# Kernel tuning notes

Hardware: AMD Instinct MI355X
Metric: run time of the kernel (lower is better)

## Reference

```python
import jax, jax.numpy as jnp
import numpy as np


def _softsign(x):
    return x / (1.0 + jnp.abs(x))


def _pad_conv3d(x, w, b):
    # replicate-pad by 1 on each spatial side, then VALID 3x3x3 conv (NCDHW)
    x = jnp.pad(x, ((0, 0), (0, 0), (1, 1), (1, 1), (1, 1)), mode='edge')
    y = jax.lax.conv_general_dilated(
        x, w, window_strides=(1, 1, 1), padding='VALID',
        dimension_numbers=('NCDHW', 'OIDHW', 'NCDHW'))
    return y + b[None, :, None, None, None]


N_MID = 100  # number of 1->1 conv blocks


def setup_inputs() -> dict:
    key = jax.random.key(0)
    ks = jax.random.split(key, 8)
    B, S = 16, 64
    preop = jax.random.normal(ks[0], (B, 1, S, S, S), dtype=jnp.float32)
    intraop = jax.random.normal(ks[1], (B, 1, S, S, S), dtype=jnp.float32)
    # conv weights: PyTorch-style kaiming-ish scale for 3x3x3 kernels
    w0 = jax.random.normal(ks[2], (1, 2, 3, 3, 3), dtype=jnp.float32) * 0.14
    b0 = jax.random.normal(ks[3], (1,), dtype=jnp.float32) * 0.05
    ws = jax.random.normal(ks[4], (N_MID, 1, 1, 3, 3, 3), dtype=jnp.float32) * 0.19
    bs = jax.random.normal(ks[5], (N_MID, 1), dtype=jnp.float32) * 0.05
    wX = jax.random.normal(ks[6], (3, 1, 3, 3, 3), dtype=jnp.float32) * 0.19
    bX = jax.random.normal(ks[7], (3,), dtype=jnp.float32) * 0.05
    return {"preoperative": preop, "intraoperative": intraop,
            "w0": w0, "b0": b0, "ws": ws, "bs": bs, "wX": wX, "bX": bX}


def reference(preoperative, intraoperative, w0, b0, ws, bs, wX, bX):
    config = jnp.concatenate((preoperative, intraoperative), axis=1)  # [B,2,D,H,W]
    h = _softsign(_pad_conv3d(config, w0, b0))  # [B,1,64,64,64]

    def step(h, wb):
        w, b = wb
        return _softsign(_pad_conv3d(h, w, b)), None

    h, _ = jax.lax.scan(step, h, (ws, bs))  # 100 chained 1->1 conv blocks
    res64 = _softsign(_pad_conv3d(h, wX, bX))  # [B,3,64,64,64]
    # torch F.interpolate default mode='nearest': src = floor(dst * in/out)
    res32 = res64[:, :, ::2, ::2, ::2]
    res16 = res64[:, :, ::4, ::4, ::4]
    res8 = res64[:, :, ::8, ::8, ::8]
    return (res64, res32, res16, res8)
```

## Files before the change

### kernel.cpp

```cpp
#include <hip/hip_runtime.h>
#include <math.h>

typedef float nfloat4 __attribute__((ext_vector_type(4), aligned(16)));
typedef float nfloat2 __attribute__((ext_vector_type(2), aligned(8)));
typedef _Float16 h16;
typedef _Float16 h4 __attribute__((ext_vector_type(4)));
typedef _Float16 h2 __attribute__((ext_vector_type(2)));

__device__ __forceinline__ float softsign(float v) {
    float d = 1.0f + fabsf(v);
    return v * __builtin_amdgcn_rcpf(d);
}
__device__ __forceinline__ void nt_store4(float* p, float a, float b, float c, float d) {
    nfloat4 v; v.x = a; v.y = b; v.z = c; v.w = d;
    __builtin_nontemporal_store(v, (nfloat4*)p);
}
__device__ __forceinline__ void nt_store2(float* p, float a, float b) {
    nfloat2 v; v.x = a; v.y = b;
    __builtin_nontemporal_store(v, (nfloat2*)p);
}
__device__ __forceinline__ int clamp63(int v) { return v < 0 ? 0 : (v > 63 ? 63 : v); }

__global__ __launch_bounds__(256) void conv_first(const float* __restrict__ in0,
                                                  const float* __restrict__ in1,
                                                  h16* __restrict__ out,
                                                  const float* __restrict__ w,
                                                  const float* __restrict__ bias) {
    int blk = blockIdx.x;
    int xcd = blk & 7;
    int j   = blk >> 3;
    int b   = j & 15;
    int z0  = (xcd << 3) + (((j >> 4) & 1) << 2);
    int y0  = ((j >> 5) & 3) << 4;
    int t = threadIdx.x;
    int xq = (t & 15) << 2;
    int y  = y0 + (t >> 4);

    const float* base0 = in0 + (size_t)b * 262144;
    const float* base1 = in1 + (size_t)b * 262144;

    float acc[4][4];
    #pragma unroll
    for (int i = 0; i < 4; ++i)
        #pragma unroll
        for (int jj = 0; jj < 4; ++jj) acc[i][jj] = 0.0f;

    #pragma unroll
    for (int zi = 0; zi < 6; ++zi) {
        int zin = clamp63(z0 + zi - 1);
        const float* p0 = base0 + zin * 4096;
        const float* p1 = base1 + zin * 4096;
        #pragma unroll
        for (int dy = 0; dy < 3; ++dy) {
            int yin = clamp63(y + dy - 1);
            const float* r0p = p0 + yin * 64;
            const float* r1p = p1 + yin * 64;
            float r0[6], r1[6];
            {
                const float4 v = *(const float4*)(r0p + xq);
                r0[0] = r0p[xq == 0 ? 0 : xq - 1];
                r0[1] = v.x; r0[2] = v.y; r0[3] = v.z; r0[4] = v.w;
                r0[5] = r0p[xq == 60 ? 63 : xq + 4];
            }
            {
                const float4 v = *(const float4*)(r1p + xq);
                r1[0] = r1p[xq == 0 ? 0 : xq - 1];
                r1[1] = v.x; r1[2] = v.y; r1[3] = v.z; r1[4] = v.w;
                r1[5] = r1p[xq == 60 ? 63 : xq + 4];
            }
            #pragma unroll
            for (int dz = 0; dz < 3; ++dz) {
                int zo = zi - dz;
                if (zo >= 0 && zo < 4) {
                    #pragma unroll
                    for (int dx = 0; dx < 3; ++dx) {
                        float w0v = w[dz * 9 + dy * 3 + dx];
                        float w1v = w[27 + dz * 9 + dy * 3 + dx];
                        #pragma unroll
                        for (int xx = 0; xx < 4; ++xx) {
                            acc[zo][xx] = fmaf(w0v, r0[xx + dx], acc[zo][xx]);
                            acc[zo][xx] = fmaf(w1v, r1[xx + dx], acc[zo][xx]);
                        }
                    }
                }
            }
        }
    }
    float bv = *bias;
    h16* obase = out + (size_t)b * 262144 + (size_t)z0 * 4096 + y * 64 + xq;
    #pragma unroll
    for (int zo = 0; zo < 4; ++zo) {
        h4 o;
        o.x = (h16)softsign(acc[zo][0] + bv);
        o.y = (h16)softsign(acc[zo][1] + bv);
        o.z = (h16)softsign(acc[zo][2] + bv);
        o.w = (h16)softsign(acc[zo][3] + bv);
        *(h4*)(obase + zo * 4096) = o;
    }
}

#define LROWH   68
#define LPLANEH 680

__global__ __launch_bounds__(256, 4) void conv_mid(const h16* __restrict__ in,
                                                   h16* __restrict__ out,
                                                   const float* __restrict__ w,
                                                   const float* __restrict__ bias) {
    __shared__ h16 lds[10 * LPLANEH];

    int blk = blockIdx.x;
    int xcd = blk & 7;
    int j   = blk >> 3;
    int b   = j & 15;
    int y0  = ((j >> 4) & 7) << 3;
    int z0  = xcd << 3;

    int t = threadIdx.x;
    int l = t & 15;
    int g = t >> 4;

    const h16* base = in + (size_t)b * 262144;

    float wv[27];
    #pragma unroll
    for (int i = 0; i < 27; ++i) wv[i] = w[i];
    float bv = *bias;

    {
        h16* lrows[7]; h4 mv[7];
        #pragma unroll
        for (int it = 0; it < 7; ++it) {
            int rid = it * 16 + g;
            int pa = rid / 10;
            pa = pa > 9 ? 9 : pa;
            int pr = rid - pa * 10;
            pr = pr > 9 ? 9 : pr;
            const h16* grow = base + clamp63(z0 - 1 + pa) * 4096 + clamp63(y0 - 1 + pr) * 64;
            lrows[it] = &lds[pa * LPLANEH + pr * LROWH];
            mv[it] = *(const h4*)(grow + 4 * l);
        }
        #pragma unroll
        for (int it = 0; it < 7; ++it) {
            int rid = it * 16 + g;
            if (rid < 100) {
                *(h4*)(lrows[it] + 4 * l) = mv[it];
                if (l == 15) {
                    h2 d; d.x = mv[it].w; d.y = mv[it].w;
                    *(h2*)(lrows[it] + 64) = d;
                }
            }
        }
    }
    __syncthreads();

    int xq   = l << 2;
    int yloc = g & 7;
    int zh   = (g >> 3) << 2;

    float acc[4][4];
    #pragma unroll
    for (int i = 0; i < 4; ++i)
        #pragma unroll
        for (int k = 0; k < 4; ++k) acc[i][k] = 0.0f;

    #pragma unroll
    for (int pp = 0; pp < 6; ++pp) {
        const h16* pl = &lds[(zh + pp) * LPLANEH];
        #pragma unroll
        for (int dy = 0; dy < 3; ++dy) {
            const h16* lrow = pl + (yloc + dy) * LROWH;
            h4 v  = *(const h4*)(lrow + xq);
            h2 v2 = *(const h2*)(lrow + xq + 4);
            h2 vf = *(const h2*)(lrow + (xq == 0 ? 0 : xq - 2));
            float r[6];
            r[0] = (xq == 0) ? (float)v.x : (float)vf.y;
            r[1] = (float)v.x; r[2] = (float)v.y; r[3] = (float)v.z;
            r[4] = (float)v.w; r[5] = (float)v2.x;
            #pragma unroll
            for (int dz = 0; dz < 3; ++dz) {
                int zz = pp - dz;
                if (zz >= 0 && zz < 4) {
                    #pragma unroll
                    for (int dx = 0; dx < 3; ++dx) {
                        float ww = wv[dz * 9 + dy * 3 + dx];
                        #pragma unroll
                        for (int xx = 0; xx < 4; ++xx)
                            acc[zz][xx] = fmaf(ww, r[xx + dx], acc[zz][xx]);
                    }
                }
            }
        }
    }

    int y = y0 + yloc;
    h16* obase = out + (size_t)b * 262144 + (size_t)(z0 + zh) * 4096 + y * 64 + xq;
    #pragma unroll
    for (int zz = 0; zz < 4; ++zz) {
        h4 o;
        o.x = (h16)softsign(acc[zz][0] + bv);
        o.y = (h16)softsign(acc[zz][1] + bv);
        o.z = (h16)softsign(acc[zz][2] + bv);
        o.w = (h16)softsign(acc[zz][3] + bv);
        *(h4*)(obase + zz * 4096) = o;
    }
}

__device__ __forceinline__ void load_row6h(const h16* __restrict__ row, int x0, float r[6]) {
    h4 v = *(const h4*)(row + x0);
    r[0] = (float)row[x0 == 0 ? 0 : x0 - 1];
    r[1] = (float)v.x; r[2] = (float)v.y; r[3] = (float)v.z; r[4] = (float)v.w;
    r[5] = (float)row[x0 == 60 ? 63 : x0 + 4];
}

__global__ __launch_bounds__(256) void conv_last(const h16* __restrict__ in,
                                                 float* __restrict__ out,
                                                 const float* __restrict__ w,
                                                 const float* __restrict__ bias) {
    int blk = blockIdx.x;
    int xcd = blk & 7;
    int j   = blk >> 3;
    int b   = j & 15;
    int z0  = (xcd << 3) + (((j >> 4) & 1) << 2);
    int y0  = ((j >> 5) & 3) << 4;
    int t = threadIdx.x;
    int xq = (t & 15) << 2;
    int y  = y0 + (t >> 4);

    const h16* base = in + (size_t)b * 262144;

    float acc[4][3][4];
    #pragma unroll
    for (int i = 0; i < 4; ++i)
        #pragma unroll
        for (int c = 0; c < 3; ++c)
            #pragma unroll
            for (int jj = 0; jj < 4; ++jj) acc[i][c][jj] = 0.0f;

    #pragma unroll
    for (int zi = 0; zi < 6; ++zi) {
        int zin = clamp63(z0 + zi - 1);
        const h16* plane = base + zin * 4096;
        #pragma unroll
        for (int dy = 0; dy < 3; ++dy) {
            int yin = clamp63(y + dy - 1);
            float r[6];
            load_row6h(plane + yin * 64, xq, r);
            #pragma unroll
            for (int dz = 0; dz < 3; ++dz) {
                int zo = zi - dz;
                if (zo >= 0 && zo < 4) {
                    #pragma unroll
                    for (int c = 0; c < 3; ++c) {
                        #pragma unroll
                        for (int dx = 0; dx < 3; ++dx) {
                            float wc = w[c * 27 + dz * 9 + dy * 3 + dx];
                            #pragma unroll
                            for (int xx = 0; xx < 4; ++xx)
                                acc[zo][c][xx] = fmaf(wc, r[xx + dx], acc[zo][c][xx]);
                        }
                    }
                }
            }
        }
    }

    float* r64 = out;
    float* r32 = out + 12582912;
    float* r16 = r32 + 1572864;
    float* r8  = r16 + 196608;

    float vals[4][3][4];
    #pragma unroll
    for (int zo = 0; zo < 4; ++zo)
        #pragma unroll
        for (int c = 0; c < 3; ++c) {
            float bv = bias[c];
            #pragma unroll
            for (int xx = 0; xx < 4; ++xx)
                vals[zo][c][xx] = softsign(acc[zo][c][xx] + bv);
        }

    #pragma unroll
    for (int c = 0; c < 3; ++c) {
        float* cb = r64 + ((size_t)b * 3 + c) * 262144 + (size_t)z0 * 4096 + y * 64 + xq;
        #pragma unroll
        for (int zo = 0; zo < 4; ++zo) {
            nt_store4(cb + zo * 4096,
                      vals[zo][c][0], vals[zo][c][1], vals[zo][c][2], vals[zo][c][3]);
        }
    }
    if ((y & 1) == 0) {
        #pragma unroll
        for (int c = 0; c < 3; ++c) {
            size_t cb = ((size_t)b * 3 + c) * 32768 + (size_t)(y >> 1) * 32;
            #pragma unroll
            for (int zo = 0; zo < 4; zo += 2) {
                size_t zb = cb + (size_t)((z0 + zo) >> 1) * 1024;
                nt_store2(r32 + zb + (xq >> 1), vals[zo][c][0], vals[zo][c][2]);
            }
        }
    }
    if ((y & 3) == 0) {
        #pragma unroll
        for (int c = 0; c < 3; ++c) {
            __builtin_nontemporal_store(vals[0][c][0],
                r16 + ((size_t)b * 3 + c) * 4096 + (size_t)(z0 >> 2) * 256 + (y >> 2) * 16 + (xq >> 2));
        }
    }
    if ((y & 7) == 0 && (z0 & 7) == 0 && (xq & 7) == 0) {
        #pragma unroll
        for (int c = 0; c < 3; ++c) {
            __builtin_nontemporal_store(vals[0][c][0],
                r8 + ((size_t)b * 3 + c) * 512 + (size_t)(z0 >> 3) * 64 + (y >> 3) * 8 + (xq >> 3));
        }
    }
}

extern "C" void kernel_launch(void* const* d_in, const int* in_sizes, int n_in,
                              void* d_out, int out_size, void* d_ws, size_t ws_size,
                              hipStream_t stream) {
    const float* preop = (const float*)d_in[0];
    const float* intra = (const float*)d_in[1];
    const float* w0    = (const float*)d_in[2];
    const float* b0p   = (const float*)d_in[3];
    const float* wsp   = (const float*)d_in[4];
    const float* bsp   = (const float*)d_in[5];
    const float* wX    = (const float*)d_in[6];
    const float* bX    = (const float*)d_in[7];
    float* out = (float*)d_out;

    h16* buf0 = (h16*)d_ws;
    h16* buf1 = (h16*)out;

    conv_first<<<dim3(1024), dim3(256), 0, stream>>>(preop, intra, buf0, w0, b0p);
    for (int i = 0; i < 100; ++i) {
        const h16* src = (i & 1) ? buf1 : buf0;
        h16* dst       = (i & 1) ? buf0 : buf1;
        conv_mid<<<dim3(1024), dim3(256), 0, stream>>>(src, dst, wsp + i * 27, bsp + i);
    }
    conv_last<<<dim3(1024), dim3(256), 0, stream>>>(buf0, out, wX, bX);
}
```

Measured before the change: 891.9 us.

## Stage conv_last input halo tile in LDS and retile blocks to 8x8 z-y

The final 3-channel conv now cooperatively loads a 10x10-row fp16 halo tile (z and y, with replicated x edge) into shared memory and computes from LDS instead of issuing repeated global row loads per thread. The block tiling changes from 4z x 16y to 8z x 8y so halo overhead is shared, and launch bounds request 4 blocks per CU. This adds a barrier and LDS traffic, and may reduce occupancy, in exchange for fewer redundant global loads.

Measured after the change: 929.0 us. +4.2%, slower.

```diff
diff --git a/kernel.cpp b/kernel.cpp
--- a/kernel.cpp
+++ b/kernel.cpp
@@ -205,50 +205,82 @@
     }
 }
 
-__device__ __forceinline__ void load_row6h(const h16* __restrict__ row, int x0, float r[6]) {
-    h4 v = *(const h4*)(row + x0);
-    r[0] = (float)row[x0 == 0 ? 0 : x0 - 1];
-    r[1] = (float)v.x; r[2] = (float)v.y; r[3] = (float)v.z; r[4] = (float)v.w;
-    r[5] = (float)row[x0 == 60 ? 63 : x0 + 4];
-}
-
-__global__ __launch_bounds__(256) void conv_last(const h16* __restrict__ in,
-                                                 float* __restrict__ out,
-                                                 const float* __restrict__ w,
-                                                 const float* __restrict__ bias) {
+__global__ __launch_bounds__(256, 4) void conv_last(const h16* __restrict__ in,
+                                                    float* __restrict__ out,
+                                                    const float* __restrict__ w,
+                                                    const float* __restrict__ bias) {
+    __shared__ h16 lds[10 * LPLANEH];
+
     int blk = blockIdx.x;
     int xcd = blk & 7;
     int j   = blk >> 3;
     int b   = j & 15;
-    int z0  = (xcd << 3) + (((j >> 4) & 1) << 2);
-    int y0  = ((j >> 5) & 3) << 4;
+    int y0  = ((j >> 4) & 7) << 3;
+    int z0  = xcd << 3;
+
     int t = threadIdx.x;
-    int xq = (t & 15) << 2;
-    int y  = y0 + (t >> 4);
+    int l = t & 15;
+    int g = t >> 4;
 
     const h16* base = in + (size_t)b * 262144;
 
+    {
+        h16* lrows[7]; h4 mv[7];
+        #pragma unroll
+        for (int it = 0; it < 7; ++it) {
+            int rid = it * 16 + g;
+            int pa = rid / 10;
+            pa = pa > 9 ? 9 : pa;
+            int pr = rid - pa * 10;
+            pr = pr > 9 ? 9 : pr;
+            const h16* grow = base + clamp63(z0 - 1 + pa) * 4096 + clamp63(y0 - 1 + pr) * 64;
+            lrows[it] = &lds[pa * LPLANEH + pr * LROWH];
+            mv[it] = *(const h4*)(grow + 4 * l);
+        }
+        #pragma unroll
+        for (int it = 0; it < 7; ++it) {
+            int rid = it * 16 + g;
+            if (rid < 100) {
+                *(h4*)(lrows[it] + 4 * l) = mv[it];
+                if (l == 15) {
+                    h2 d; d.x = mv[it].w; d.y = mv[it].w;
+                    *(h2*)(lrows[it] + 64) = d;
+                }
+            }
+        }
+    }
+    __syncthreads();
+
+    int xq   = l << 2;
+    int yloc = g & 7;
+    int zh   = (g >> 3) << 2;
+    int zq   = z0 + zh;
+
     float acc[4][3][4];
     #pragma unroll
     for (int i = 0; i < 4; ++i)
         #pragma unroll
         for (int c = 0; c < 3; ++c)
             #pragma unroll
-            for (int jj = 0; jj < 4; ++jj) acc[i][c][jj] = 0.0f;
-
-    #pragma unroll
-    for (int zi = 0; zi < 6; ++zi) {
-        int zin = clamp63(z0 + zi - 1);
-        const h16* plane = base + zin * 4096;
+            for (int k = 0; k < 4; ++k) acc[i][c][k] = 0.0f;
+
+    #pragma unroll
+    for (int pp = 0; pp < 6; ++pp) {
+        const h16* pl = &lds[(zh + pp) * LPLANEH];
         #pragma unroll
         for (int dy = 0; dy < 3; ++dy) {
-            int yin = clamp63(y + dy - 1);
+            const h16* lrow = pl + (yloc + dy) * LROWH;
+            h4 v  = *(const h4*)(lrow + xq);
+            h2 v2 = *(const h2*)(lrow + xq + 4);
+            h2 vf = *(const h2*)(lrow + (xq == 0 ? 0 : xq - 2));
             float r[6];
-            load_row6h(plane + yin * 64, xq, r);
+            r[0] = (xq == 0) ? (float)v.x : (float)vf.y;
+            r[1] = (float)v.x; r[2] = (float)v.y; r[3] = (float)v.z;
+            r[4] = (float)v.w; r[5] = (float)v2.x;
             #pragma unroll
             for (int dz = 0; dz < 3; ++dz) {
-                int zo = zi - dz;
-                if (zo >= 0 && zo < 4) {
+                int zz = pp - dz;
+                if (zz >= 0 && zz < 4) {
                     #pragma unroll
                     for (int c = 0; c < 3; ++c) {
                         #pragma unroll
@@ -256,20 +288,21 @@
                             float wc = w[c * 27 + dz * 9 + dy * 3 + dx];
                             #pragma unroll
                             for (int xx = 0; xx < 4; ++xx)
-                                acc[zo][c][xx] = fmaf(wc, r[xx + dx], acc[zo][c][xx]);
+                                acc[zz][c][xx] = fmaf(wc, r[xx + dx], acc[zz][c][xx]);
                         }
                     }
                 }
             }
         }
     }
+
+    int y = y0 + yloc;
 
     float* r64 = out;
     float* r32 = out + 12582912;
     float* r16 = r32 + 1572864;
     float* r8  = r16 + 196608;
 
-    float vals[4][3][4];
     #pragma unroll
     for (int zo = 0; zo < 4; ++zo)
         #pragma unroll
@@ -277,16 +310,16 @@
             float bv = bias[c];
             #pragma unroll
             for (int xx = 0; xx < 4; ++xx)
-                vals[zo][c][xx] = softsign(acc[zo][c][xx] + bv);
+                acc[zo][c][xx] = softsign(acc[zo][c][xx] + bv);
         }
 
     #pragma unroll
     for (int c = 0; c < 3; ++c) {
-        float* cb = r64 + ((size_t)b * 3 + c) * 262144 + (size_t)z0 * 4096 + y * 64 + xq;
+        float* cb = r64 + ((size_t)b * 3 + c) * 262144 + (size_t)zq * 4096 + y * 64 + xq;
         #pragma unroll
         for (int zo = 0; zo < 4; ++zo) {
             nt_store4(cb + zo * 4096,
-                      vals[zo][c][0], vals[zo][c][1], vals[zo][c][2], vals[zo][c][3]);
+                      acc[zo][c][0], acc[zo][c][1], acc[zo][c][2], acc[zo][c][3]);
         }
     }
     if ((y & 1) == 0) {
@@ -295,23 +328,23 @@
             size_t cb = ((size_t)b * 3 + c) * 32768 + (size_t)(y >> 1) * 32;
             #pragma unroll
             for (int zo = 0; zo < 4; zo += 2) {
-                size_t zb = cb + (size_t)((z0 + zo) >> 1) * 1024;
-                nt_store2(r32 + zb + (xq >> 1), vals[zo][c][0], vals[zo][c][2]);
+                size_t zb = cb + (size_t)((zq + zo) >> 1) * 1024;
+                nt_store2(r32 + zb + (xq >> 1), acc[zo][c][0], acc[zo][c][2]);
             }
         }
     }
     if ((y & 3) == 0) {
         #pragma unroll
         for (int c = 0; c < 3; ++c) {
-            __builtin_nontemporal_store(vals[0][c][0],
-                r16 + ((size_t)b * 3 + c) * 4096 + (size_t)(z0 >> 2) * 256 + (y >> 2) * 16 + (xq >> 2));
-        }
-    }
-    if ((y & 7) == 0 && (z0 & 7) == 0 && (xq & 7) == 0) {
+            __builtin_nontemporal_store(acc[0][c][0],
+                r16 + ((size_t)b * 3 + c) * 4096 + (size_t)(zq >> 2) * 256 + (y >> 2) * 16 + (xq >> 2));
+        }
+    }
+    if ((y & 7) == 0 && (zq & 7) == 0 && (xq & 7) == 0) {
         #pragma unroll
         for (int c = 0; c < 3; ++c) {
-            __builtin_nontemporal_store(vals[0][c][0],
-                r8 + ((size_t)b * 3 + c) * 512 + (size_t)(z0 >> 3) * 64 + (y >> 3) * 8 + (xq >> 3));
+            __builtin_nontemporal_store(acc[0][c][0],
+                r8 + ((size_t)b * 3 + c) * 512 + (size_t)(zq >> 3) * 64 + (y >> 3) * 8 + (xq >> 3));
         }
     }
 }
```
